# Performance work log

Measured on AMD Instinct MI355X. Metric: run time of the kernel, lower is better.

The kernel has to match this reference:

```python
import jax, jax.numpy as jnp
import numpy as np

GRID_SIZE = 5
SPLINE_ORDER = 3
NUM_BASIS = GRID_SIZE + SPLINE_ORDER  # 8


def _make_grid(in_features):
    # efficient-kan style uniform extended grid over [-1, 1]
    h = 2.0 / GRID_SIZE
    g = jnp.arange(-SPLINE_ORDER, GRID_SIZE + SPLINE_ORDER + 1, dtype=jnp.float32) * h - 1.0
    return jnp.broadcast_to(g, (in_features, g.shape[0]))  # [in, 12]


def _b_splines(x, grid):
    # x: [..., in], grid: [in, G]; returns [..., in, NUM_BASIS] via Cox-de Boor
    xe = x[..., None]
    bases = ((xe >= grid[:, :-1]) & (xe < grid[:, 1:])).astype(x.dtype)
    for k in range(1, SPLINE_ORDER + 1):
        left = (xe - grid[:, :-(k + 1)]) / (grid[:, k:-1] - grid[:, :-(k + 1)]) * bases[..., :-1]
        right = (grid[:, k + 1:] - xe) / (grid[:, k + 1:] - grid[:, 1:-k]) * bases[..., 1:]
        bases = left + right
    return bases


def kan_linear(x, bw, sw):
    # bw: [out, in], sw: [out, in, NUM_BASIS]
    base = jnp.matmul(jax.nn.silu(x), bw.T)
    spl = _b_splines(x, _make_grid(bw.shape[1]))
    spline = jnp.einsum('...ik,oik->...o', spl, sw)
    return base + spline


def kan2(x, bw1, sw1, bw2, sw2):
    return kan_linear(kan_linear(x, bw1, sw1), bw2, sw2)


def _att_matrix(q, bw1, sw1, bw2, sw2):
    n, h = q.shape
    pairs = jnp.concatenate([
        jnp.broadcast_to(q[:, None, :], (n, n, h)),
        jnp.broadcast_to(q[None, :, :], (n, n, h)),
    ], axis=-1)  # [n, n, 2h]
    return kan2(pairs, bw1, sw1, bw2, sw2)[..., 0]  # [n, n]


def setup_inputs() -> dict:
    key = jax.random.key(0)
    ks = jax.random.split(key, 32)
    n, h, m = 384, 32, 50

    def rn(k, shape, s=1.0):
        return jax.random.normal(k, shape, dtype=jnp.float32) * s

    inp = {
        'x': rn(ks[0], (n, h)),
        'y': rn(ks[1], (n, h)),
        'target': rn(ks[2], (n, h)),
        'bias': rn(ks[3], (1,), 0.1),
    }
    i = 4
    for pre in ('x', 'y', 't'):
        din = 2 * h
        inp[pre + '1bw'] = rn(ks[i], (m, din), 0.1)
        inp[pre + '1sw'] = rn(ks[i + 1], (m, din, NUM_BASIS), 0.1)
        inp[pre + '2bw'] = rn(ks[i + 2], (1, m), 0.1)
        inp[pre + '2sw'] = rn(ks[i + 3], (1, m, NUM_BASIS), 0.1)
        i += 4
    inp['f1bw'] = rn(ks[i], (m, 3 * h), 0.1)
    inp['f1sw'] = rn(ks[i + 1], (m, 3 * h, NUM_BASIS), 0.1)
    inp['f2bw'] = rn(ks[i + 2], (3, m), 0.1)
    inp['f2sw'] = rn(ks[i + 3], (3, m, NUM_BASIS), 0.1)
    i += 4
    inp['l1bw'] = rn(ks[i], (h, h), 0.1)
    inp['l1sw'] = rn(ks[i + 1], (h, h, NUM_BASIS), 0.1)
    inp['l2bw'] = rn(ks[i + 2], (h, h), 0.1)
    inp['l2sw'] = rn(ks[i + 3], (h, h, NUM_BASIS), 0.1)
    return inp


def reference(x, y, target, bias,
              x1bw, x1sw, x2bw, x2sw,
              y1bw, y1sw, y2bw, y2sw,
              t1bw, t1sw, t2bw, t2sw,
              f1bw, f1sw, f2bw, f2sw,
              l1bw, l1sw, l2bw, l2sw):
    xA = _att_matrix(x, x1bw, x1sw, x2bw, x2sw)
    yA = _att_matrix(y, y1bw, y1sw, y2bw, y2sw)
    tA = _att_matrix(target, t1bw, t1sw, t2bw, t2sw)

    # dynamic modal fusion weights
    feats = jnp.concatenate([x.mean(0, keepdims=True), y.mean(0, keepdims=True),
                             target.mean(0, keepdims=True)], axis=-1)  # [1, 3h]
    w = jax.nn.softmax(kan2(feats, f1bw, f1sw, f2bw, f2sw), axis=-1)[0]  # [3]

    fusion_att = w[0] * xA + w[1] * yA + w[2] * tA + bias
    fusion_att = jax.nn.softmax(fusion_att, axis=-1)
    target_att = jnp.matmul(fusion_att, target)  # dropout is identity at eval
    y1 = jax.nn.relu(kan_linear(target_att, l1bw, l1sw))
    y2 = jax.nn.relu(kan_linear(y1, l2bw, l2sw))
    return y2
```

## Files before the change

### kernel.cpp

```cpp
#include <hip/hip_runtime.h>

#define NN 384
#define HH 32
#define MM 50

__device__ __forceinline__ float fastRcp(float x) { return __builtin_amdgcn_rcpf(x); }

__device__ __forceinline__ void featEval(float x, float& sil, int& kb, float b[4]) {
  sil = x * fastRcp(1.0f + __expf(-x));
  const float u  = (x + 1.0f) * 2.5f;
  const float fu = floorf(u);
  const bool valid = (fu >= -3.0f) && (fu <= 7.0f);
  const float s = valid ? (1.0f / 6.0f) : 0.0f;
  kb = valid ? (int)fu : 100;
  const float tt = u - fu;
  const float t2 = tt * tt, t3 = t2 * tt, omt = 1.0f - tt;
  b[0] = omt * omt * omt * s;
  b[1] = (3.0f * t3 - 6.0f * t2 + 4.0f) * s;
  b[2] = (-3.0f * t3 + 3.0f * t2 + 3.0f * tt + 1.0f) * s;
  b[3] = t3 * s;
}

__device__ __forceinline__ float waveReduce(float v) {
#pragma unroll
  for (int off = 32; off > 0; off >>= 1) v += __shfl_down(v, off);
  return v;
}

__device__ __forceinline__ float dot4(float4 a, float4 b) {
  float r = a.x * b.x;
  r = fmaf(a.y, b.y, r);
  r = fmaf(a.z, b.z, r);
  r = fmaf(a.w, b.w, r);
  return r;
}

__global__ __launch_bounds__(384) void stageA_kernel(
    const float* __restrict__ x, const float* __restrict__ y, const float* __restrict__ tg,
    const float* __restrict__ xbw, const float* __restrict__ xsw,
    const float* __restrict__ ybw, const float* __restrict__ ysw,
    const float* __restrict__ tbw, const float* __restrict__ tsw,
    const float* __restrict__ f1bw, const float* __restrict__ f1sw,
    const float* __restrict__ f2bw, const float* __restrict__ f2sw,
    float* __restrict__ A, float* __restrict__ Bt, float* __restrict__ wout)
{
  const int tid = threadIdx.x;
  const int lane = tid & 63, w = tid >> 6;
  const int i = blockIdx.x;
  const int m = blockIdx.y;
  const int half = blockIdx.z;

  if (i < NN) {
    __shared__ float bas[HH * 8];
    __shared__ float sil[HH];
    const float* q  = (m == 0) ? x   : ((m == 1) ? y   : tg);
    const float* bw = (m == 0) ? xbw : ((m == 1) ? ybw : tbw);
    const float* sw = (m == 0) ? xsw : ((m == 1) ? ysw : tsw);
    const int cb = half * HH;

    if (tid < HH * 8) bas[tid] = 0.0f;
    __syncthreads();
    if (tid < HH) {
      float b[4]; float s; int kb;
      featEval(q[i * HH + tid], s, kb, b);
      sil[tid] = s;
#pragma unroll
      for (int r = 0; r < 4; ++r) {
        const int k = kb + r;
        if ((unsigned)k < 8u) bas[tid * 8 + k] = b[r];
      }
    }
    __syncthreads();

    const float4* bas4 = (const float4*)bas;
    const float4 bb = bas4[lane];
    for (int o = w; o < MM; o += 6) {
      const float4* sp4 = (const float4*)(sw + ((size_t)(o * 2 * HH + cb) << 3));
      float acc = dot4(sp4[lane], bb);
      if (lane < HH)
        acc = fmaf(bw[o * 2 * HH + cb + lane], sil[lane], acc);
      acc = waveReduce(acc);
      if (lane == 0) {
        if (half == 0) A[((size_t)m * NN + i) * MM + o] = acc;
        else           Bt[((size_t)m * MM + o) * NN + i] = acc;
      }
    }
    return;
  }

  if (m != 0 || half != 0) return;
  {
    __shared__ float4 part4[3][8][16];
    __shared__ float sil96[96];
    __shared__ float bas768[96 * 8];
    __shared__ float z1[MM];
    __shared__ float sil2[MM];
    __shared__ float bas400[MM * 8];
    __shared__ float s3[3];

    {
      const int mm = tid >> 7;
      const int sub = tid & 127;
      const int q4 = sub >> 4;
      const int prt = sub & 15;
      const float* src = (mm == 0) ? x : ((mm == 1) ? y : tg);
      const float4* s4 = (const float4*)src;
      float4 a = make_float4(0.f, 0.f, 0.f, 0.f);
      for (int r = prt; r < NN; r += 16) {
        const float4 v = s4[r * 8 + q4];
        a.x += v.x; a.y += v.y; a.z += v.z; a.w += v.w;
      }
      part4[mm][q4][prt] = a;
    }
    for (int idx = tid; idx < 96 * 8; idx += 384) bas768[idx] = 0.0f;
    for (int idx = tid; idx < MM * 8; idx += 384) bas400[idx] = 0.0f;
    __syncthreads();

    if (tid < 96) {
      const int mm = tid >> 5, col = tid & 31;
      const int q4 = col >> 2, comp = col & 3;
      const float* pp = (const float*)&part4[mm][q4][0];
      float v = 0.0f;
#pragma unroll
      for (int prt = 0; prt < 16; ++prt) v += pp[prt * 4 + comp];
      const float fv = v * (1.0f / NN);
      float b[4]; float s; int kb;
      featEval(fv, s, kb, b);
      sil96[tid] = s;
#pragma unroll
      for (int r = 0; r < 4; ++r) {
        const int k = kb + r;
        if ((unsigned)k < 8u) bas768[tid * 8 + k] = b[r];
      }
    }
    __syncthreads();

    {
      const float4* bas4 = (const float4*)bas768;
      for (int o = w; o < MM; o += 6) {
        const float4* sp4 = (const float4*)(f1sw + (size_t)o * (96 * 8));
        float acc = 0.0f;
#pragma unroll
        for (int r = 0; r < 3; ++r)
          acc += dot4(sp4[lane + 64 * r], bas4[lane + 64 * r]);
#pragma unroll
        for (int r = 0; r < 2; ++r) {
          const int e = lane + 64 * r;
          if (e < 96) acc = fmaf(f1bw[o * 96 + e], sil96[e], acc);
        }
        acc = waveReduce(acc);
        if (lane == 0) z1[o] = acc;
      }
    }
    __syncthreads();

    if (tid < MM) {
      float b[4]; float s; int kb;
      featEval(z1[tid], s, kb, b);
      sil2[tid] = s;
#pragma unroll
      for (int r = 0; r < 4; ++r) {
        const int k = kb + r;
        if ((unsigned)k < 8u) bas400[tid * 8 + k] = b[r];
      }
    }
    __syncthreads();

    if (w < 3) {
      const float4* bas4 = (const float4*)bas400;
      const float4* sp4 = (const float4*)(f2sw + (size_t)w * (MM * 8));
      float acc = 0.0f;
#pragma unroll
      for (int r = 0; r < 2; ++r) {
        const int f = lane + 64 * r;
        if (f < MM * 2) acc += dot4(sp4[f], bas4[f]);
      }
      if (lane < MM) acc = fmaf(f2bw[w * MM + lane], sil2[lane], acc);
      acc = waveReduce(acc);
      if (lane == 0) s3[w] = acc;
    }
    __syncthreads();

    if (tid == 0) {
      const float mx = fmaxf(s3[0], fmaxf(s3[1], s3[2]));
      const float e0 = __expf(s3[0] - mx), e1 = __expf(s3[1] - mx), e2 = __expf(s3[2] - mx);
      const float inv = fastRcp(e0 + e1 + e2);
      wout[0] = e0 * inv; wout[1] = e1 * inv; wout[2] = e2 * inv;
    }
  }
}

__global__ __launch_bounds__(384) void score_kernel(
    const float* __restrict__ A, const float* __restrict__ Bt,
    const float* __restrict__ x2bw, const float* __restrict__ y2bw, const float* __restrict__ t2bw,
    const float* __restrict__ x2sw, const float* __restrict__ y2sw, const float* __restrict__ t2sw,
    float* __restrict__ Sp)
{
  __shared__ float sA[MM];
  __shared__ float sBW[MM];
  __shared__ float pad[MM][14];
  __shared__ float4 coef[MM][13];
  const int tid = threadIdx.x;
  const int i = blockIdx.x;
  const int m = blockIdx.y;
  const float* bsrc = (m == 0) ? x2bw : ((m == 1) ? y2bw : t2bw);
  const float* ssrc = (m == 0) ? x2sw : ((m == 1) ? y2sw : t2sw);

  for (int idx = tid; idx < MM * 6; idx += 384) {
    const int kk = idx / 6, r = idx - kk * 6;
    pad[kk][(r < 3) ? r : (r + 8)] = 0.0f;
  }
  for (int idx = tid; idx < MM * 8; idx += 384) {
    pad[idx >> 3][3 + (idx & 7)] = ssrc[idx];
  }
  if (tid < MM) {
    sA[tid]  = A[((size_t)m * NN + i) * MM + tid];
    sBW[tid] = bsrc[tid];
  }
  __syncthreads();

  for (int idx = tid; idx < MM * 11; idx += 384) {
    const int k = idx / 11, cm1 = idx - k * 11;
    const float* bp = &pad[k][cm1];
    const float p0 = bp[0], p1 = bp[1], p2 = bp[2], p3 = bp[3];
    const float a0 = (p0 + 4.0f * p1 + p2) * (1.0f / 6.0f);
    const float a1 = (p2 - p0) * 0.5f;
    const float a2 = (p0 - 2.0f * p1 + p2) * 0.5f;
    const float a3 = (p3 - p0) * (1.0f / 6.0f) + (p1 - p2) * 0.5f;
    coef[k][cm1 + 1] = make_float4(a0, a1, a2, a3);
  }
  if (tid < MM * 2) {
    coef[tid >> 1][(tid & 1) * 12] = make_float4(0.f, 0.f, 0.f, 0.f);
  }
  __syncthreads();

  const float* BtBase = Bt + (size_t)m * MM * NN + tid;
  float acc0 = 0.0f, acc1 = 0.0f;
  for (int k = 0; k < MM; k += 2) {
    const float z0 = sA[k]     + BtBase[(size_t)k * NN];
    const float z1 = sA[k + 1] + BtBase[(size_t)(k + 1) * NN];
    {
      const float u = fmaf(z0, 2.5f, 2.5f);
      const float fu = floorf(u);
      const float t = u - fu;
      const int cc = (int)(fminf(fmaxf(fu, -4.0f), 8.0f)) + 4;
      const float4 C = coef[k][cc];
      acc0 += fmaf(t, fmaf(t, fmaf(t, C.w, C.z), C.y), C.x);
      const float sg = fastRcp(1.0f + __expf(-z0));
      acc0 = fmaf(z0 * sg, sBW[k], acc0);
    }
    {
      const float u = fmaf(z1, 2.5f, 2.5f);
      const float fu = floorf(u);
      const float t = u - fu;
      const int cc = (int)(fminf(fmaxf(fu, -4.0f), 8.0f)) + 4;
      const float4 C = coef[k + 1][cc];
      acc1 += fmaf(t, fmaf(t, fmaf(t, C.w, C.z), C.y), C.x);
      const float sg = fastRcp(1.0f + __expf(-z1));
      acc1 = fmaf(z1 * sg, sBW[k + 1], acc1);
    }
  }
  Sp[((size_t)m * NN + i) * NN + tid] = acc0 + acc1;
}

__global__ __launch_bounds__(384) void row_kernel(
    const float* __restrict__ Sp, const float* __restrict__ wv, const float* __restrict__ bias,
    const float* __restrict__ tg,
    const float* __restrict__ l1bw, const float* __restrict__ l1sw,
    const float* __restrict__ l2bw, const float* __restrict__ l2sw,
    float* __restrict__ out)
{
  __shared__ float p[NN];
  __shared__ float redm[6], reds[6];
  __shared__ float part[12][HH];
  __shared__ float ta[HH];
  __shared__ float basF[HH * 8];
  __shared__ float silF[HH];
  __shared__ float y1v[HH];
  const int tid = threadIdx.x;
  const int lane = tid & 63, w = tid >> 6;
  const int i = blockIdx.x;

  float stot = bias[0];
  stot = fmaf(wv[0], Sp[(size_t)i * NN + tid], stot);
  stot = fmaf(wv[1], Sp[((size_t)NN + i) * NN + tid], stot);
  stot = fmaf(wv[2], Sp[((size_t)2 * NN + i) * NN + tid], stot);

  float v = stot;
#pragma unroll
  for (int off = 32; off > 0; off >>= 1) v = fmaxf(v, __shfl_down(v, off));
  if (lane == 0) redm[w] = v;
  __syncthreads();
  float mx = redm[0];
#pragma unroll
  for (int ww = 1; ww < 6; ++ww) mx = fmaxf(mx, redm[ww]);
  const float e = __expf(stot - mx);
  p[tid] = e;
  float sv = e;
#pragma unroll
  for (int off = 32; off > 0; off >>= 1) sv += __shfl_down(sv, off);
  if (lane == 0) reds[w] = sv;
  __syncthreads();
  const float ssum = reds[0] + reds[1] + reds[2] + reds[3] + reds[4] + reds[5];
  const float inv = 1.0f / ssum;

  const int d = tid & 31, g = tid >> 5;
  float acc2 = 0.0f;
  for (int s2 = 0; s2 < 32; ++s2) {
    const int j = g * 32 + s2;
    acc2 = fmaf(p[j], tg[j * HH + d], acc2);
  }
  part[g][d] = acc2;
  if (tid < HH * 8) basF[tid] = 0.0f;
  __syncthreads();
  if (tid < HH) {
    float a = 0.0f;
#pragma unroll
    for (int gg = 0; gg < 12; ++gg) a += part[gg][tid];
    ta[tid] = a * inv;
  }
  __syncthreads();

  if (tid < HH) {
    float b[4]; float s; int kb;
    featEval(ta[tid], s, kb, b);
    silF[tid] = s;
#pragma unroll
    for (int r = 0; r < 4; ++r) {
      const int k = kb + r;
      if ((unsigned)k < 8u) basF[tid * 8 + k] = b[r];
    }
  }
  __syncthreads();
  {
    const float4 bb = ((const float4*)basF)[lane];
    for (int o = w; o < HH; o += 6) {
      const float4* sp4 = (const float4*)(l1sw + ((size_t)o << 8));
      float acc = dot4(sp4[lane], bb);
      if (lane < HH) acc = fmaf(l1bw[o * HH + lane], silF[lane], acc);
      acc = waveReduce(acc);
      if (lane == 0) y1v[o] = fmaxf(acc, 0.0f);
    }
  }
  __syncthreads();
  if (tid < HH * 8) basF[tid] = 0.0f;
  __syncthreads();
  if (tid < HH) {
    float b[4]; float s; int kb;
    featEval(y1v[tid], s, kb, b);
    silF[tid] = s;
#pragma unroll
    for (int r = 0; r < 4; ++r) {
      const int k = kb + r;
      if ((unsigned)k < 8u) basF[tid * 8 + k] = b[r];
    }
  }
  __syncthreads();
  {
    const float4 bb = ((const float4*)basF)[lane];
    for (int o = w; o < HH; o += 6) {
      const float4* sp4 = (const float4*)(l2sw + ((size_t)o << 8));
      float acc = dot4(sp4[lane], bb);
      if (lane < HH) acc = fmaf(l2bw[o * HH + lane], silF[lane], acc);
      acc = waveReduce(acc);
      if (lane == 0) out[i * HH + o] = fmaxf(acc, 0.0f);
    }
  }
}

extern "C" void kernel_launch(void* const* d_in, const int* in_sizes, int n_in,
                              void* d_out, int out_size, void* d_ws, size_t ws_size,
                              hipStream_t stream)
{
  const float* x    = (const float*)d_in[0];
  const float* y    = (const float*)d_in[1];
  const float* tg   = (const float*)d_in[2];
  const float* bias = (const float*)d_in[3];
  const float* x1bw = (const float*)d_in[4];
  const float* x1sw = (const float*)d_in[5];
  const float* x2bw = (const float*)d_in[6];
  const float* x2sw = (const float*)d_in[7];
  const float* y1bw = (const float*)d_in[8];
  const float* y1sw = (const float*)d_in[9];
  const float* y2bw = (const float*)d_in[10];
  const float* y2sw = (const float*)d_in[11];
  const float* t1bw = (const float*)d_in[12];
  const float* t1sw = (const float*)d_in[13];
  const float* t2bw = (const float*)d_in[14];
  const float* t2sw = (const float*)d_in[15];
  const float* f1bw = (const float*)d_in[16];
  const float* f1sw = (const float*)d_in[17];
  const float* f2bw = (const float*)d_in[18];
  const float* f2sw = (const float*)d_in[19];
  const float* l1bw = (const float*)d_in[20];
  const float* l1sw = (const float*)d_in[21];
  const float* l2bw = (const float*)d_in[22];
  const float* l2sw = (const float*)d_in[23];
  float* out = (float*)d_out;

  float* ws = (float*)d_ws;
  float* A  = ws;
  float* Bt = ws + 3 * NN * MM;
  float* Sp = ws + 6 * NN * MM;
  float* wv = Sp + 3 * NN * NN;

  stageA_kernel<<<dim3(NN + 1, 3, 2), 384, 0, stream>>>(
      x, y, tg, x1bw, x1sw, y1bw, y1sw, t1bw, t1sw,
      f1bw, f1sw, f2bw, f2sw, A, Bt, wv);
  score_kernel<<<dim3(NN, 3), 384, 0, stream>>>(A, Bt, x2bw, y2bw, t2bw,
                                                x2sw, y2sw, t2sw, Sp);
  row_kernel<<<NN, 384, 0, stream>>>(Sp, wv, bias, tg, l1bw, l1sw, l2bw, l2sw, out);
}
```

Measured before the change: 48.62 us.

## Process two query rows per block in stageA and score kernels

Each block in the stageA and score kernels now handles two rows i instead of one. The spline weight and base weight loads, the Bt column loads and the per-block coefficient table setup are shared across both rows, and both grids are halved. The score loop also prefetches the next pair of Bt values and is unrolled. In exchange there are fewer blocks, so parallelism is lower, and register pressure rises.

New measurement: 52.23 us. 1.07x slower.

```diff
diff --git a/kernel.cpp b/kernel.cpp
--- a/kernel.cpp
+++ b/kernel.cpp
@@ -46,43 +46,55 @@
 {
   const int tid = threadIdx.x;
   const int lane = tid & 63, w = tid >> 6;
-  const int i = blockIdx.x;
+  const int bi = blockIdx.x;
   const int m = blockIdx.y;
   const int half = blockIdx.z;
 
-  if (i < NN) {
-    __shared__ float bas[HH * 8];
-    __shared__ float sil[HH];
+  if (bi < NN / 2) {
+    __shared__ float bas[2][HH * 8];
+    __shared__ float sil[2][HH];
+    const int i0 = bi * 2;
     const float* q  = (m == 0) ? x   : ((m == 1) ? y   : tg);
     const float* bw = (m == 0) ? xbw : ((m == 1) ? ybw : tbw);
     const float* sw = (m == 0) ? xsw : ((m == 1) ? ysw : tsw);
     const int cb = half * HH;
 
-    if (tid < HH * 8) bas[tid] = 0.0f;
-    __syncthreads();
-    if (tid < HH) {
+    for (int idx = tid; idx < 2 * HH * 8; idx += 384) (&bas[0][0])[idx] = 0.0f;
+    __syncthreads();
+    if (tid < 2 * HH) {
+      const int r = tid >> 5, d = tid & 31;
       float b[4]; float s; int kb;
-      featEval(q[i * HH + tid], s, kb, b);
-      sil[tid] = s;
-#pragma unroll
-      for (int r = 0; r < 4; ++r) {
-        const int k = kb + r;
-        if ((unsigned)k < 8u) bas[tid * 8 + k] = b[r];
-      }
-    }
-    __syncthreads();
-
-    const float4* bas4 = (const float4*)bas;
-    const float4 bb = bas4[lane];
+      featEval(q[(i0 + r) * HH + d], s, kb, b);
+      sil[r][d] = s;
+#pragma unroll
+      for (int rr = 0; rr < 4; ++rr) {
+        const int k = kb + rr;
+        if ((unsigned)k < 8u) bas[r][d * 8 + k] = b[rr];
+      }
+    }
+    __syncthreads();
+
+    const float4 bb0 = ((const float4*)&bas[0][0])[lane];
+    const float4 bb1 = ((const float4*)&bas[1][0])[lane];
+    const float sl0 = (lane < HH) ? sil[0][lane] : 0.0f;
+    const float sl1 = (lane < HH) ? sil[1][lane] : 0.0f;
     for (int o = w; o < MM; o += 6) {
-      const float4* sp4 = (const float4*)(sw + ((size_t)(o * 2 * HH + cb) << 3));
-      float acc = dot4(sp4[lane], bb);
-      if (lane < HH)
-        acc = fmaf(bw[o * 2 * HH + cb + lane], sil[lane], acc);
-      acc = waveReduce(acc);
+      const float4 wv4 = ((const float4*)(sw + ((size_t)(o * 2 * HH + cb) << 3)))[lane];
+      const float bwv = (lane < HH) ? bw[o * 2 * HH + cb + lane] : 0.0f;
+      float a0 = dot4(wv4, bb0);
+      float a1 = dot4(wv4, bb1);
+      a0 = fmaf(bwv, sl0, a0);
+      a1 = fmaf(bwv, sl1, a1);
+      a0 = waveReduce(a0);
+      a1 = waveReduce(a1);
       if (lane == 0) {
-        if (half == 0) A[((size_t)m * NN + i) * MM + o] = acc;
-        else           Bt[((size_t)m * MM + o) * NN + i] = acc;
+        if (half == 0) {
+          A[((size_t)m * NN + i0) * MM + o]     = a0;
+          A[((size_t)m * NN + i0 + 1) * MM + o] = a1;
+        } else {
+          Bt[((size_t)m * MM + o) * NN + i0]     = a0;
+          Bt[((size_t)m * MM + o) * NN + i0 + 1] = a1;
+        }
       }
     }
     return;
@@ -196,13 +208,14 @@
     const float* __restrict__ x2sw, const float* __restrict__ y2sw, const float* __restrict__ t2sw,
     float* __restrict__ Sp)
 {
-  __shared__ float sA[MM];
+  __shared__ float sA[2][MM];
   __shared__ float sBW[MM];
   __shared__ float pad[MM][14];
   __shared__ float4 coef[MM][13];
   const int tid = threadIdx.x;
-  const int i = blockIdx.x;
+  const int ii = blockIdx.x;
   const int m = blockIdx.y;
+  const int i0 = ii * 2;
   const float* bsrc = (m == 0) ? x2bw : ((m == 1) ? y2bw : t2bw);
   const float* ssrc = (m == 0) ? x2sw : ((m == 1) ? y2sw : t2sw);
 
@@ -213,9 +226,11 @@
   for (int idx = tid; idx < MM * 8; idx += 384) {
     pad[idx >> 3][3 + (idx & 7)] = ssrc[idx];
   }
-  if (tid < MM) {
-    sA[tid]  = A[((size_t)m * NN + i) * MM + tid];
-    sBW[tid] = bsrc[tid];
+  if (tid < 2 * MM) {
+    const int r = (tid >= MM) ? 1 : 0;
+    const int k = tid - r * MM;
+    sA[r][k] = A[((size_t)m * NN + i0 + r) * MM + k];
+    if (r == 0) sBW[k] = bsrc[k];
   }
   __syncthreads();
 
@@ -235,32 +250,40 @@
   __syncthreads();
 
   const float* BtBase = Bt + (size_t)m * MM * NN + tid;
-  float acc0 = 0.0f, acc1 = 0.0f;
+  float acc00 = 0.0f, acc01 = 0.0f, acc10 = 0.0f, acc11 = 0.0f;
+  float za = BtBase[0];
+  float zb = BtBase[NN];
+
+#define KAN_EVAL(zz, kk, accv)                                          \
+  {                                                                     \
+    const float z_ = (zz);                                              \
+    const float u_ = fmaf(z_, 2.5f, 2.5f);                              \
+    const float fu_ = floorf(u_);                                       \
+    const float t_ = u_ - fu_;                                          \
+    const int cc_ = (int)(fminf(fmaxf(fu_, -4.0f), 8.0f)) + 4;          \
+    const float4 C_ = coef[kk][cc_];                                    \
+    accv += fmaf(t_, fmaf(t_, fmaf(t_, C_.w, C_.z), C_.y), C_.x);       \
+    const float sg_ = fastRcp(1.0f + __expf(-z_));                      \
+    accv = fmaf(z_ * sg_, sBW[kk], accv);                               \
+  }
+
+#pragma unroll 5
   for (int k = 0; k < MM; k += 2) {
-    const float z0 = sA[k]     + BtBase[(size_t)k * NN];
-    const float z1 = sA[k + 1] + BtBase[(size_t)(k + 1) * NN];
-    {
-      const float u = fmaf(z0, 2.5f, 2.5f);
-      const float fu = floorf(u);
-      const float t = u - fu;
-      const int cc = (int)(fminf(fmaxf(fu, -4.0f), 8.0f)) + 4;
-      const float4 C = coef[k][cc];
-      acc0 += fmaf(t, fmaf(t, fmaf(t, C.w, C.z), C.y), C.x);
-      const float sg = fastRcp(1.0f + __expf(-z0));
-      acc0 = fmaf(z0 * sg, sBW[k], acc0);
-    }
-    {
-      const float u = fmaf(z1, 2.5f, 2.5f);
-      const float fu = floorf(u);
-      const float t = u - fu;
-      const int cc = (int)(fminf(fmaxf(fu, -4.0f), 8.0f)) + 4;
-      const float4 C = coef[k + 1][cc];
-      acc1 += fmaf(t, fmaf(t, fmaf(t, C.w, C.z), C.y), C.x);
-      const float sg = fastRcp(1.0f + __expf(-z1));
-      acc1 = fmaf(z1 * sg, sBW[k + 1], acc1);
-    }
-  }
-  Sp[((size_t)m * NN + i) * NN + tid] = acc0 + acc1;
+    float zc = 0.0f, zd = 0.0f;
+    if (k + 3 < MM) {
+      zc = BtBase[(size_t)(k + 2) * NN];
+      zd = BtBase[(size_t)(k + 3) * NN];
+    }
+    KAN_EVAL(sA[0][k] + za,     k,     acc00);
+    KAN_EVAL(sA[1][k] + za,     k,     acc10);
+    KAN_EVAL(sA[0][k + 1] + zb, k + 1, acc01);
+    KAN_EVAL(sA[1][k + 1] + zb, k + 1, acc11);
+    za = zc; zb = zd;
+  }
+#undef KAN_EVAL
+
+  Sp[((size_t)m * NN + i0) * NN + tid]     = acc00 + acc01;
+  Sp[((size_t)m * NN + i0 + 1) * NN + tid] = acc10 + acc11;
 }
 
 __global__ __launch_bounds__(384) void row_kernel(
@@ -404,10 +427,10 @@
   float* Sp = ws + 6 * NN * MM;
   float* wv = Sp + 3 * NN * NN;
 
-  stageA_kernel<<<dim3(NN + 1, 3, 2), 384, 0, stream>>>(
+  stageA_kernel<<<dim3(NN / 2 + 1, 3, 2), 384, 0, stream>>>(
       x, y, tg, x1bw, x1sw, y1bw, y1sw, t1bw, t1sw,
       f1bw, f1sw, f2bw, f2sw, A, Bt, wv);
-  score_kernel<<<dim3(NN, 3), 384, 0, stream>>>(A, Bt, x2bw, y2bw, t2bw,
-                                                x2sw, y2sw, t2sw, Sp);
+  score_kernel<<<dim3(NN / 2, 3), 384, 0, stream>>>(A, Bt, x2bw, y2bw, t2bw,
+                                                    x2sw, y2sw, t2sw, Sp);
   row_kernel<<<NN, 384, 0, stream>>>(Sp, wv, bias, tg, l1bw, l1sw, l2bw, l2sw, out);
 }
```
